# Kernel optimization log

Hardware: AMD Instinct MI355X
Metric: run time of the kernel (lower is better)

The kernel has to match this reference:

```python
import jax, jax.numpy as jnp
import numpy as np
import math

B, H, T, N = 2, 4, 2048, 2048
THETA = 2.0 ** 16


def get_freqs(n: int, theta: float) -> jnp.ndarray:
    # quantize arange to multiples of 2, matching torch (t/2).floor()*2
    t = jnp.arange(n, dtype=jnp.float32)
    q = jnp.floor(t / 2.0) * 2.0
    return 1.0 / theta ** (q / n) / (2.0 * math.pi)


def rope(phases: jnp.ndarray, v: jnp.ndarray) -> jnp.ndarray:
    # v: [B,H,T,N]; phases: [T,N] (broadcast). Interleaved pair rotation.
    ph = (phases % 1.0) * (2.0 * math.pi)
    c, s = jnp.cos(ph), jnp.sin(ph)
    v2 = v.reshape(*v.shape[:-1], -1, 2)           # [...,N/2,2]
    v_rot = jnp.stack((-v2[..., 1], v2[..., 0]), axis=-1).reshape(v.shape)
    return (v * c + v_rot * s).astype(v.dtype)


def setup_inputs() -> dict:
    key = jax.random.key(0)
    kq, kv = jax.random.split(key)
    Q = jax.random.normal(kq, (B, H, T, N), dtype=jnp.float32)
    V = jax.random.normal(kv, (B, H, T, N), dtype=jnp.float32)
    return {"Q": Q, "V": V}


def reference(Q, V):
    Tlen = Q.shape[2]
    n = Q.shape[3]
    freqs = get_freqs(n, THETA)                               # [N]
    phases = jnp.arange(Tlen, dtype=jnp.float32)[:, None] * freqs[None, :]  # [T,N]
    QR = rope(phases, Q)                                      # K is Q -> KR = QR
    scores = jnp.einsum('bhtn,bhsn->bhts', QR, QR)            # [B,H,T,T]
    # strictly-causal mask: keep s < t (tril with diagonal=-1)
    mask = jnp.tril(jnp.ones((Tlen, Tlen), dtype=bool), k=-1)
    scores = jnp.where(mask, scores, 0.0)
    out = jnp.einsum('bhts,bhsn->bhtn', scores, V)
    return out
```

## Files before the change

### kernel.cpp

```cpp
#include <hip/hip_runtime.h>
#include <hip/hip_bf16.h>

#define TDIM 2048
#define NDIM 2048
#define BHN  8
#define LD   2048

typedef __attribute__((ext_vector_type(8))) short bf16x8;
typedef __attribute__((ext_vector_type(4))) float f32x4;
typedef unsigned short us;

template <int N> struct ic { static constexpr int v = N; };

static __device__ __forceinline__ us f2bf(float x) {
  union { __hip_bfloat16 h; us u; } cv;
  cv.h = __float2bfloat16(x);
  return cv.u;
}

__global__ __launch_bounds__(256) void rope_kernel(const float* __restrict__ Q,
                                                   us* __restrict__ QR,
                                                   int total8) {
  int idx = blockIdx.x * blockDim.x + threadIdx.x;
  if (idx >= total8) return;
  long base = (long)idx * 8;
  int n = (int)(base & (NDIM - 1));
  int t = (int)((base >> 11) & (TDIM - 1));
  const float4* p = reinterpret_cast<const float4*>(Q + base);
  float4 v0 = p[0], v1 = p[1];
  float q[8] = {v0.x, v0.y, v0.z, v0.w, v1.x, v1.y, v1.z, v1.w};
  us r[8];
  float tf = (float)t;
#pragma unroll
  for (int pr = 0; pr < 4; ++pr) {
    int nn = n + pr * 2;
    float freq = __builtin_exp2f((float)nn * (-1.0f / 128.0f)) * 0.15915494309189535f;
    float ph = tf * freq;
    ph = ph - __builtin_floorf(ph);
    float c = __builtin_amdgcn_cosf(ph);
    float s = __builtin_amdgcn_sinf(ph);
    float e = q[2 * pr], o = q[2 * pr + 1];
    r[2 * pr]     = f2bf(e * c - o * s);
    r[2 * pr + 1] = f2bf(o * c + e * s);
  }
  union { us usv[8]; bf16x8 v; } pk;
#pragma unroll
  for (int i = 0; i < 8; ++i) pk.usv[i] = r[i];
  *reinterpret_cast<bf16x8*>(QR + base) = pk.v;
}

__global__ __launch_bounds__(256) void vtrans_kernel(const float* __restrict__ V,
                                                     us* __restrict__ VT,
                                                     us* __restrict__ Sflag) {
  __shared__ float tile[64 * 66];
  if (Sflag != nullptr && blockIdx.x == 0 && blockIdx.y == 0 && blockIdx.z == 0 &&
      threadIdx.x == 0) {
    for (int h = 0; h < BHN; ++h) {
      unsigned* f = (unsigned*)(Sflag + (long)h * TDIM * LD + 1792);
      for (int i = 0; i < 40; ++i)
        __hip_atomic_store(&f[i], 0u, __ATOMIC_RELAXED, __HIP_MEMORY_SCOPE_AGENT);
    }
  }
  const int bh = blockIdx.z;
  const int t0 = blockIdx.x * 64, n0 = blockIdx.y * 64;
  const float* Vp = V + (long)bh * TDIM * NDIM;
  us* Tp = VT + (long)bh * TDIM * NDIM;
  const int tid = (int)threadIdx.x;
  {
    const int tx4 = tid & 15, ty = tid >> 4;
#pragma unroll
    for (int i = 0; i < 4; ++i) {
      int row = ty + i * 16;
      float4 v = *reinterpret_cast<const float4*>(
          Vp + (long)(t0 + row) * NDIM + n0 + tx4 * 4);
      float* d = &tile[row * 66 + tx4 * 4];
      d[0] = v.x; d[1] = v.y; d[2] = v.z; d[3] = v.w;
    }
  }
  __syncthreads();
  {
    const int sx = tid & 15, sy = tid >> 4;
#pragma unroll
    for (int j = 0; j < 4; ++j) {
      int n = sy * 4 + j;
      unsigned r0 = f2bf(tile[(sx * 4 + 0) * 66 + n]);
      unsigned r1 = f2bf(tile[(sx * 4 + 1) * 66 + n]);
      unsigned r2 = f2bf(tile[(sx * 4 + 2) * 66 + n]);
      unsigned r3 = f2bf(tile[(sx * 4 + 3) * 66 + n]);
      uint2 val;
      val.x = r0 | (r1 << 16);
      val.y = r2 | (r3 << 16);
      *reinterpret_cast<uint2*>(Tp + (long)(n0 + n) * TDIM + t0 + sx * 4) = val;
    }
  }
}

template <int PASS>
__device__ __forceinline__ void run_tile(const us* __restrict__ A,
                                         const us* __restrict__ B,
                                         void* __restrict__ Cbase,
                                         us* __restrict__ lds,
                                         int rt, int ct, int tid,
                                         unsigned* __restrict__ fh) {
  const int lane = tid & 63, wid = tid >> 6;
  const int wr = wid >> 2, wc = wid & 3;
  const int l15 = lane & 15, l4 = lane >> 4;
  const int row0 = rt * 256, col0 = ct * 256;
  const int kts = (PASS == 0) ? 32 : (rt + 1) * 4;
  const int fbase = rt * (rt + 1) / 2;

  f32x4 acc[8][4];
#pragma unroll
  for (int m = 0; m < 8; ++m)
#pragma unroll
    for (int n = 0; n < 4; ++n) acc[m][n] = (f32x4){0.f, 0.f, 0.f, 0.f};

  auto stage = [&](int half , int t) {
    const us* g0 = (half < 2) ? A : B;
    const int tr0 = (half < 2) ? row0 : col0;
    const int h = half & 1;
    us* lb = lds + ((half < 2) ? 0 : 32768) + (t & 1) * 16384;
    const int k0 = t * 64;
#pragma unroll
    for (int r = 0; r < 2; ++r) {
      int off = r * 512 + tid;
      int row = off >> 3;
      int ch = off & 7;
      int chl = ch ^ (row & 7);
      const us* g = g0 + (long)(tr0 + h * 128 + row) * LD + (k0 + chl * 8);
      us* l = lb + h * 8192 + off * 8;
      __builtin_amdgcn_global_load_lds(
          (const __attribute__((address_space(1))) unsigned int*)g,
          (__attribute__((address_space(3))) unsigned int*)l, 16, 0, 0);
    }
  };
  auto ldA = [&](int b, int m, int ks) -> bf16x8 {
    int row = wr * 128 + m * 16 + l15;
    int ch = (ks * 4 + l4) ^ (row & 7);
    return *reinterpret_cast<const bf16x8*>(lds + b * 16384 + row * 64 + ch * 8);
  };
  auto ldB = [&](int b, int n, int ks) -> bf16x8 {
    int row = wc * 64 + n * 16 + l15;
    int ch = (ks * 4 + l4) ^ (row & 7);
    return *reinterpret_cast<const bf16x8*>(lds + 32768 + b * 16384 + row * 64 + ch * 8);
  };

  if constexpr (PASS == 1) {
    stage(2, 0); stage(3, 0);
    if (wid == 0) {
      unsigned need = (1u << (rt + 1)) - 1u;
      for (;;) {
        unsigned ok = 0;
        if (lane <= rt)
          ok = (__hip_atomic_fetch_add(&fh[fbase + lane], 0u, __ATOMIC_RELAXED,
                                       __HIP_MEMORY_SCOPE_AGENT) != 0u);
        unsigned long long m = __ballot(ok);
        if (((unsigned)m & need) == need) break;
        __builtin_amdgcn_s_sleep(8);
      }
    }
    __builtin_amdgcn_s_barrier();
    asm volatile("" ::: "memory");
    stage(0, 0); stage(1, 0);
    if (1 < kts) { stage(2, 1); stage(3, 1); }
  } else {
    stage(0, 0); stage(1, 0); stage(2, 0); stage(3, 0);
    if (1 < kts) { stage(2, 1); stage(3, 1); }
  }
  asm volatile("s_waitcnt vmcnt(4)" ::: "memory");
  __builtin_amdgcn_s_barrier();
  __builtin_amdgcn_sched_barrier(0);

  bf16x8 af[4][2], bfr[4][2];
  auto kstep = [&](int t, auto bbc) {
    constexpr int b = decltype(bbc)::v;
#pragma unroll
    for (int m = 0; m < 4; ++m) { af[m][0] = ldA(b, m, 0); af[m][1] = ldA(b, m, 1); }
#pragma unroll
    for (int n = 0; n < 2; ++n) { bfr[n][0] = ldB(b, n, 0); bfr[n][1] = ldB(b, n, 1); }
    if (t + 1 < kts) stage(0, t + 1);
    __builtin_amdgcn_s_barrier();
    asm volatile("s_waitcnt lgkmcnt(0)" ::: "memory");
    __builtin_amdgcn_sched_barrier(0);
    __builtin_amdgcn_s_setprio(1);
#pragma unroll
    for (int m = 0; m < 4; ++m)
#pragma unroll
      for (int n = 0; n < 2; ++n)
#pragma unroll
        for (int ks = 0; ks < 2; ++ks)
          acc[m][n] = __builtin_amdgcn_mfma_f32_16x16x32_bf16(af[m][ks], bfr[n][ks], acc[m][n], 0, 0, 0);
    __builtin_amdgcn_s_setprio(0);
    __builtin_amdgcn_sched_barrier(0);
    __builtin_amdgcn_s_barrier();
#pragma unroll
    for (int n = 2; n < 4; ++n) { bfr[n][0] = ldB(b, n, 0); bfr[n][1] = ldB(b, n, 1); }
    if (t + 1 < kts) stage(1, t + 1);
    __builtin_amdgcn_s_barrier();
    asm volatile("s_waitcnt lgkmcnt(0)" ::: "memory");
    __builtin_amdgcn_sched_barrier(0);
    __builtin_amdgcn_s_setprio(1);
#pragma unroll
    for (int m = 0; m < 4; ++m)
#pragma unroll
      for (int n = 2; n < 4; ++n)
#pragma unroll
        for (int ks = 0; ks < 2; ++ks)
          acc[m][n] = __builtin_amdgcn_mfma_f32_16x16x32_bf16(af[m][ks], bfr[n][ks], acc[m][n], 0, 0, 0);
    __builtin_amdgcn_s_setprio(0);
    __builtin_amdgcn_sched_barrier(0);
    __builtin_amdgcn_s_barrier();
#pragma unroll
    for (int m = 0; m < 4; ++m) { af[m][0] = ldA(b, m + 4, 0); af[m][1] = ldA(b, m + 4, 1); }
    if (t + 2 < kts) stage(2, t + 2);
    __builtin_amdgcn_s_barrier();
    asm volatile("s_waitcnt lgkmcnt(0)" ::: "memory");
    __builtin_amdgcn_sched_barrier(0);
    __builtin_amdgcn_s_setprio(1);
#pragma unroll
    for (int m = 0; m < 4; ++m)
#pragma unroll
      for (int n = 0; n < 2; ++n)
#pragma unroll
        for (int ks = 0; ks < 2; ++ks)
          acc[m + 4][n] = __builtin_amdgcn_mfma_f32_16x16x32_bf16(af[m][ks], bfr[n][ks], acc[m + 4][n], 0, 0, 0);
    __builtin_amdgcn_s_setprio(0);
    __builtin_amdgcn_sched_barrier(0);
    __builtin_amdgcn_s_barrier();
    if (t + 2 < kts) stage(3, t + 2);
    __builtin_amdgcn_s_setprio(1);
#pragma unroll
    for (int m = 0; m < 4; ++m)
#pragma unroll
      for (int n = 2; n < 4; ++n)
#pragma unroll
        for (int ks = 0; ks < 2; ++ks)
          acc[m + 4][n] = __builtin_amdgcn_mfma_f32_16x16x32_bf16(af[m][ks], bfr[n][ks], acc[m + 4][n], 0, 0, 0);
    __builtin_amdgcn_s_setprio(0);
    if (t + 2 < kts) { asm volatile("s_waitcnt vmcnt(4)" ::: "memory"); }
    else             { asm volatile("s_waitcnt vmcnt(0)" ::: "memory"); }
    __builtin_amdgcn_sched_barrier(0);
    __builtin_amdgcn_s_barrier();
    __builtin_amdgcn_sched_barrier(0);
  };
  for (int t = 0; t < kts; t += 2) {
    kstep(t, ic<0>{});
    kstep(t + 1, ic<1>{});
  }

  if constexpr (PASS == 0) {
    us* C = (us*)Cbase;
    const bool diag = (rt == ct);
#pragma unroll
    for (int m = 0; m < 8; ++m) {
      int r0 = row0 + wr * 128 + m * 16 + l4 * 4;
#pragma unroll
      for (int n = 0; n < 4; ++n) {
        int cc = col0 + wc * 64 + n * 16 + l15;
#pragma unroll
        for (int j = 0; j < 4; ++j) {
          int tt = r0 + j;
          float v = acc[m][n][j];
          if (diag && cc >= tt) v = 0.0f;
          C[(long)tt * LD + cc] = f2bf(v);
        }
      }
    }
    __syncthreads();
    if (tid == 0)
      __hip_atomic_store(&fh[fbase + ct], 1u, __ATOMIC_RELEASE,
                         __HIP_MEMORY_SCOPE_AGENT);
  } else {
    float* C = (float*)Cbase;
#pragma unroll
    for (int m = 0; m < 8; ++m) {
      int r0 = row0 + wr * 128 + m * 16 + l4 * 4;
#pragma unroll
      for (int n = 0; n < 4; ++n) {
        int cc = col0 + wc * 64 + n * 16 + l15;
#pragma unroll
        for (int j = 0; j < 4; ++j)
          C[(long)(r0 + j) * LD + cc] = acc[m][n][j];
      }
    }
  }
}

__global__ __launch_bounds__(512, 2) void gemm_fused(const us* __restrict__ QR,
                                                     const us* __restrict__ VT,
                                                     us* __restrict__ S,
                                                     float* __restrict__ Out) {
  extern __shared__ us lds[];
  const int b = (int)blockIdx.x;
  const int head = b & 7, u = b >> 3;
  const int tid = (int)threadIdx.x;
  const us* QRh = QR + (long)head * TDIM * LD;
  const us* VTh = VT + (long)head * TDIM * LD;
  us* Sh = S + (long)head * TDIM * LD;
  float* Oh = Out + (long)head * TDIM * LD;
  unsigned* fh = (unsigned*)(Sh + 1792);
  unsigned* qc = fh + 36;

  int rt0, ct0;
  if (u < 8)       { rt0 = 7; ct0 = u; }
  else if (u < 15) { rt0 = 6; ct0 = u - 8; }
  else if (u < 21) { rt0 = 5; ct0 = u - 15; }
  else if (u < 26) { rt0 = 4; ct0 = u - 21; }
  else if (u < 30) { rt0 = 3; ct0 = u - 26; }
  else             { rt0 = 2; ct0 = (u == 30) ? 0 : 2; }
  run_tile<0>(QRh, QRh, Sh, lds, rt0, ct0, tid, fh);
  if (u >= 28) {
    int rt1, ct1;
    if (u == 28)      { rt1 = 1; ct1 = 0; }
    else if (u == 29) { rt1 = 1; ct1 = 1; }
    else if (u == 30) { rt1 = 2; ct1 = 1; }
    else              { rt1 = 0; ct1 = 0; }
    run_tile<0>(QRh, QRh, Sh, lds, rt1, ct1, tid, fh);
    run_tile<1>(Sh, VTh, Oh, lds, 1, u - 28, tid, fh);
  }

  for (;;) {
    if (tid == 0) {
      unsigned i = __hip_atomic_fetch_add(qc, 1u, __ATOMIC_RELAXED,
                                          __HIP_MEMORY_SCOPE_AGENT);
      *(volatile unsigned*)lds = i;
    }
    __syncthreads();
    unsigned i = *(volatile unsigned*)lds;
    __syncthreads();
    if (i >= 60) break;
    int rt, ct;
    if (i < 48)      { rt = 7 - (int)(i >> 3); ct = (int)(i & 7); }
    else if (i < 52) { rt = 1; ct = (int)(i - 44); }
    else             { rt = 0; ct = (int)(i - 52); }
    run_tile<1>(Sh, VTh, Oh, lds, rt, ct, tid, fh);
  }
}

template <int PASS>
__global__ __launch_bounds__(512, 2) void gemm256(
    const us* __restrict__ Abase, const us* __restrict__ Bbase,
    void* __restrict__ Cbase, int nh) {
  extern __shared__ us lds[];
  int bid = (int)blockIdx.x;
  int head, rt = 0, ct, cls = 0;
  if constexpr (PASS == 0) {
    head = bid % nh;
    int tri = bid / nh;
    rt = 0;
    while ((rt + 1) * (rt + 2) / 2 <= tri) ++rt;
    ct = tri - rt * (rt + 1) / 2;
  } else {
    head = bid % nh;
    int rem = bid / nh;
    ct = rem & 7;
    cls = rem >> 3;
  }
  const us* A = Abase + (long)head * TDIM * LD;
  const us* B = Bbase + (long)head * TDIM * LD;
  us* Sh = (us*)Cbase + (long)head * TDIM * LD;
  const int tid = (int)threadIdx.x;
  const int NSEG = (PASS == 0) ? 1 : 2;
#pragma unroll 1
  for (int seg = 0; seg < NSEG; ++seg) {
    int rts = rt, cts = ct;
    if constexpr (PASS == 1) { rts = seg ? cls : 7 - cls; cts = ct; }
    if constexpr (PASS == 0) {
      run_tile<0>(A, A, Sh, lds, rts, cts, tid, (unsigned*)(Sh + 1792));
    } else {
      float* Oh = (float*)Cbase + (long)head * TDIM * LD;
      run_tile<1>(A, B, Oh, lds, rts, cts, tid,
                  (unsigned*)((us*)Abase + (long)head * TDIM * LD + 1792));
    }
  }
}

extern "C" void kernel_launch(void* const* d_in, const int* in_sizes, int n_in,
                              void* d_out, int out_size, void* d_ws, size_t ws_size,
                              hipStream_t stream) {
  const float* Q = (const float*)d_in[0];
  const float* V = (const float*)d_in[1];
  float* Out = (float*)d_out;
  char* ws = (char*)d_ws;
  const long TN = (long)TDIM * NDIM;
  const size_t BUF = (size_t)BHN * TN * 2;
  const size_t PERBH = (size_t)TN * 2;
  const int SHMEM = 131072;

  hipFuncSetAttribute(reinterpret_cast<const void*>(&gemm_fused),
                      hipFuncAttributeMaxDynamicSharedMemorySize, SHMEM);
  hipFuncSetAttribute(reinterpret_cast<const void*>(&gemm256<0>),
                      hipFuncAttributeMaxDynamicSharedMemorySize, SHMEM);
  hipFuncSetAttribute(reinterpret_cast<const void*>(&gemm256<1>),
                      hipFuncAttributeMaxDynamicSharedMemorySize, SHMEM);

  if (ws_size >= 3 * BUF) {
    us* QRb = (us*)ws;
    us* VbT = (us*)(ws + BUF);
    us* S   = (us*)(ws + 2 * BUF);
    int total8 = (int)(BHN * TN / 8);
    rope_kernel<<<dim3(total8 / 256), dim3(256), 0, stream>>>(Q, QRb, total8);
    vtrans_kernel<<<dim3(32, 32, 8), dim3(256), 0, stream>>>(V, VbT, S);
    void* args[] = {(void*)&QRb, (void*)&VbT, (void*)&S, (void*)&Out};
    hipError_t ce = hipLaunchCooperativeKernel(
        reinterpret_cast<const void*>(&gemm_fused), dim3(256), dim3(512),
        args, (unsigned)SHMEM, stream);
    if (ce != hipSuccess) {
      (void)hipGetLastError();
      gemm256<0><<<dim3(36 * BHN), dim3(512), SHMEM, stream>>>(QRb, QRb, S, BHN);
      gemm256<1><<<dim3(32 * BHN), dim3(512), SHMEM, stream>>>(S, VbT, Out, BHN);
    }
  } else {
    us* QR0 = (us*)ws;
    us* VT0 = (us*)(ws + PERBH);
    us* S0  = (us*)(ws + 2 * PERBH);
    int total8 = (int)(TN / 8);
    for (int bh = 0; bh < BHN; ++bh) {
      rope_kernel<<<dim3(total8 / 256), dim3(256), 0, stream>>>(Q + bh * TN, QR0, total8);
      vtrans_kernel<<<dim3(32, 32, 1), dim3(256), 0, stream>>>(V + bh * TN, VT0, S0);
      gemm256<0><<<dim3(36), dim3(512), SHMEM, stream>>>(QR0, QR0, S0, 1);
      gemm256<1><<<dim3(32), dim3(512), SHMEM, stream>>>(S0, VT0, Out + bh * TN, 1);
    }
  }
}
```

Before: 280.2 us.

## Prefetch work-queue index during tile and move flag wait before staging

The persistent PV loop now fetches the next work-queue index with an atomic while the current tile runs. The index is stored in a dedicated LDS slot, which grows shared memory by 16 bytes, so the atomic latency is hidden behind compute. The dependency-flag spin wait for pass 1 moves to the start of the tile, so the V-tile prefetch no longer overlaps the wait. The k-loop is also rewritten from a compile-time double-buffer lambda into a runtime loop that uses `t & 1` as the buffer index. This drops constant-folded LDS addressing and may add address arithmetic.

```diff
diff --git a/kernel.cpp b/kernel.cpp
--- a/kernel.cpp
+++ b/kernel.cpp
@@ -9,8 +9,6 @@
 typedef __attribute__((ext_vector_type(8))) short bf16x8;
 typedef __attribute__((ext_vector_type(4))) float f32x4;
 typedef unsigned short us;
-
-template <int N> struct ic { static constexpr int v = N; };
 
 static __device__ __forceinline__ us f2bf(float x) {
   union { __hip_bfloat16 h; us u; } cv;
@@ -109,6 +107,23 @@
   const int kts = (PASS == 0) ? 32 : (rt + 1) * 4;
   const int fbase = rt * (rt + 1) / 2;
 
+  if constexpr (PASS == 1) {
+    if (wid == 0) {
+      unsigned need = (1u << (rt + 1)) - 1u;
+      for (;;) {
+        unsigned ok = 0;
+        if (lane <= rt)
+          ok = (__hip_atomic_fetch_add(&fh[fbase + lane], 0u, __ATOMIC_RELAXED,
+                                       __HIP_MEMORY_SCOPE_AGENT) != 0u);
+        unsigned long long m = __ballot(ok);
+        if (((unsigned)m & need) == need) break;
+        __builtin_amdgcn_s_sleep(8);
+      }
+    }
+    __builtin_amdgcn_s_barrier();
+    asm volatile("" ::: "memory");
+  }
+
   f32x4 acc[8][4];
 #pragma unroll
   for (int m = 0; m < 8; ++m)
@@ -145,35 +160,15 @@
     return *reinterpret_cast<const bf16x8*>(lds + 32768 + b * 16384 + row * 64 + ch * 8);
   };
 
-  if constexpr (PASS == 1) {
-    stage(2, 0); stage(3, 0);
-    if (wid == 0) {
-      unsigned need = (1u << (rt + 1)) - 1u;
-      for (;;) {
-        unsigned ok = 0;
-        if (lane <= rt)
-          ok = (__hip_atomic_fetch_add(&fh[fbase + lane], 0u, __ATOMIC_RELAXED,
-                                       __HIP_MEMORY_SCOPE_AGENT) != 0u);
-        unsigned long long m = __ballot(ok);
-        if (((unsigned)m & need) == need) break;
-        __builtin_amdgcn_s_sleep(8);
-      }
-    }
-    __builtin_amdgcn_s_barrier();
-    asm volatile("" ::: "memory");
-    stage(0, 0); stage(1, 0);
-    if (1 < kts) { stage(2, 1); stage(3, 1); }
-  } else {
-    stage(0, 0); stage(1, 0); stage(2, 0); stage(3, 0);
-    if (1 < kts) { stage(2, 1); stage(3, 1); }
-  }
+  stage(0, 0); stage(1, 0); stage(2, 0); stage(3, 0);
+  if (1 < kts) { stage(2, 1); stage(3, 1); }
   asm volatile("s_waitcnt vmcnt(4)" ::: "memory");
   __builtin_amdgcn_s_barrier();
   __builtin_amdgcn_sched_barrier(0);
 
   bf16x8 af[4][2], bfr[4][2];
-  auto kstep = [&](int t, auto bbc) {
-    constexpr int b = decltype(bbc)::v;
+  for (int t = 0; t < kts; ++t) {
+    const int b = t & 1;
 #pragma unroll
     for (int m = 0; m < 4; ++m) { af[m][0] = ldA(b, m, 0); af[m][1] = ldA(b, m, 1); }
 #pragma unroll
@@ -242,10 +237,6 @@
     __builtin_amdgcn_sched_barrier(0);
     __builtin_amdgcn_s_barrier();
     __builtin_amdgcn_sched_barrier(0);
-  };
-  for (int t = 0; t < kts; t += 2) {
-    kstep(t, ic<0>{});
-    kstep(t + 1, ic<1>{});
   }
 
   if constexpr (PASS == 0) {
@@ -300,6 +291,7 @@
   float* Oh = Out + (long)head * TDIM * LD;
   unsigned* fh = (unsigned*)(Sh + 1792);
   unsigned* qc = fh + 36;
+  volatile unsigned* qslot = (volatile unsigned*)(lds + 65536);
 
   int rt0, ct0;
   if (u < 8)       { rt0 = 7; ct0 = u; }
@@ -319,21 +311,28 @@
     run_tile<1>(Sh, VTh, Oh, lds, 1, u - 28, tid, fh);
   }
 
-  for (;;) {
+  if (tid == 0) {
+    unsigned i = __hip_atomic_fetch_add(qc, 1u, __ATOMIC_RELAXED,
+                                        __HIP_MEMORY_SCOPE_AGENT);
+    *qslot = i;
+  }
+  __syncthreads();
+  unsigned icur = *qslot;
+  __syncthreads();
+  while (icur < 60) {
     if (tid == 0) {
       unsigned i = __hip_atomic_fetch_add(qc, 1u, __ATOMIC_RELAXED,
                                           __HIP_MEMORY_SCOPE_AGENT);
-      *(volatile unsigned*)lds = i;
-    }
+      *qslot = i;
+    }
+    int rt, ct;
+    if (icur < 48)      { rt = 7 - (int)(icur >> 3); ct = (int)(icur & 7); }
+    else if (icur < 52) { rt = 1; ct = (int)(icur - 44); }
+    else                { rt = 0; ct = (int)(icur - 52); }
+    run_tile<1>(Sh, VTh, Oh, lds, rt, ct, tid, fh);
     __syncthreads();
-    unsigned i = *(volatile unsigned*)lds;
+    icur = *qslot;
     __syncthreads();
-    if (i >= 60) break;
-    int rt, ct;
-    if (i < 48)      { rt = 7 - (int)(i >> 3); ct = (int)(i & 7); }
-    else if (i < 52) { rt = 1; ct = (int)(i - 44); }
-    else             { rt = 0; ct = (int)(i - 52); }
-    run_tile<1>(Sh, VTh, Oh, lds, rt, ct, tid, fh);
   }
 }
 
@@ -385,7 +384,7 @@
   const long TN = (long)TDIM * NDIM;
   const size_t BUF = (size_t)BHN * TN * 2;
   const size_t PERBH = (size_t)TN * 2;
-  const int SHMEM = 131072;
+  const int SHMEM = 131088;
 
   hipFuncSetAttribute(reinterpret_cast<const void*>(&gemm_fused),
                       hipFuncAttributeMaxDynamicSharedMemorySize, SHMEM);
```

Result: no change. 282.6 us (+0.9%).

## Merge rope and V-transpose into one prep kernel and simplify GEMM k-loop

Applied to the files above, without the earlier changes.

Combines the rope and V-transpose kernels into a single prep launch that dispatches blocks by index, removing one launch and the gap between them. In the GEMM tile, the pass-1 flag wait now happens before any staging instead of overlapping with the B-tile prefetch. The manually unrolled two-step kstep lambda with compile-time buffer index is also replaced by a plain loop with a runtime buffer index. The later flag wait and runtime LDS indexing may cost some latency hiding and add address arithmetic.

```diff
diff --git a/kernel.cpp b/kernel.cpp
--- a/kernel.cpp
+++ b/kernel.cpp
@@ -10,20 +10,15 @@
 typedef __attribute__((ext_vector_type(4))) float f32x4;
 typedef unsigned short us;
 
-template <int N> struct ic { static constexpr int v = N; };
-
 static __device__ __forceinline__ us f2bf(float x) {
   union { __hip_bfloat16 h; us u; } cv;
   cv.h = __float2bfloat16(x);
   return cv.u;
 }
 
-__global__ __launch_bounds__(256) void rope_kernel(const float* __restrict__ Q,
-                                                   us* __restrict__ QR,
-                                                   int total8) {
-  int idx = blockIdx.x * blockDim.x + threadIdx.x;
-  if (idx >= total8) return;
-  long base = (long)idx * 8;
+static __device__ __forceinline__ void rope_unit(const float* __restrict__ Q,
+                                                 us* __restrict__ QR, long idx) {
+  long base = idx * 8;
   int n = (int)(base & (NDIM - 1));
   int t = (int)((base >> 11) & (TDIM - 1));
   const float4* p = reinterpret_cast<const float4*>(Q + base);
@@ -49,23 +44,10 @@
   *reinterpret_cast<bf16x8*>(QR + base) = pk.v;
 }
 
-__global__ __launch_bounds__(256) void vtrans_kernel(const float* __restrict__ V,
-                                                     us* __restrict__ VT,
-                                                     us* __restrict__ Sflag) {
-  __shared__ float tile[64 * 66];
-  if (Sflag != nullptr && blockIdx.x == 0 && blockIdx.y == 0 && blockIdx.z == 0 &&
-      threadIdx.x == 0) {
-    for (int h = 0; h < BHN; ++h) {
-      unsigned* f = (unsigned*)(Sflag + (long)h * TDIM * LD + 1792);
-      for (int i = 0; i < 40; ++i)
-        __hip_atomic_store(&f[i], 0u, __ATOMIC_RELAXED, __HIP_MEMORY_SCOPE_AGENT);
-    }
-  }
-  const int bh = blockIdx.z;
-  const int t0 = blockIdx.x * 64, n0 = blockIdx.y * 64;
-  const float* Vp = V + (long)bh * TDIM * NDIM;
-  us* Tp = VT + (long)bh * TDIM * NDIM;
-  const int tid = (int)threadIdx.x;
+static __device__ __forceinline__ void vtrans_tile(const float* __restrict__ Vp,
+                                                   us* __restrict__ Tp,
+                                                   float* __restrict__ tile,
+                                                   int t0, int n0, int tid) {
   {
     const int tx4 = tid & 15, ty = tid >> 4;
 #pragma unroll
@@ -93,6 +75,34 @@
       *reinterpret_cast<uint2*>(Tp + (long)(n0 + n) * TDIM + t0 + sx * 4) = val;
     }
   }
+}
+
+__global__ __launch_bounds__(256) void prep_kernel(const float* __restrict__ Q,
+                                                   const float* __restrict__ V,
+                                                   us* __restrict__ QR,
+                                                   us* __restrict__ VT,
+                                                   us* __restrict__ Sflag,
+                                                   int nh) {
+  __shared__ float tile[64 * 66];
+  const int bid = (int)blockIdx.x;
+  const int tid = (int)threadIdx.x;
+  const int nrope = nh * 2048;
+  if (bid == 0 && tid == 0) {
+    for (int h = 0; h < nh; ++h) {
+      unsigned* f = (unsigned*)(Sflag + (long)h * TDIM * LD + 1792);
+      for (int i = 0; i < 40; ++i)
+        __hip_atomic_store(&f[i], 0u, __ATOMIC_RELAXED, __HIP_MEMORY_SCOPE_AGENT);
+    }
+  }
+  if (bid < nrope) {
+    rope_unit(Q, QR, (long)bid * 256 + tid);
+    return;
+  }
+  const int vb = bid - nrope;
+  const int bh = vb >> 10;
+  const int rem = vb & 1023;
+  vtrans_tile(V + (long)bh * TDIM * NDIM, VT + (long)bh * TDIM * NDIM, tile,
+              (rem & 31) * 64, (rem >> 5) * 64, tid);
 }
 
 template <int PASS>
@@ -109,6 +119,23 @@
   const int kts = (PASS == 0) ? 32 : (rt + 1) * 4;
   const int fbase = rt * (rt + 1) / 2;
 
+  if constexpr (PASS == 1) {
+    if (wid == 0) {
+      unsigned need = (1u << (rt + 1)) - 1u;
+      for (;;) {
+        unsigned ok = 0;
+        if (lane <= rt)
+          ok = (__hip_atomic_fetch_add(&fh[fbase + lane], 0u, __ATOMIC_RELAXED,
+                                       __HIP_MEMORY_SCOPE_AGENT) != 0u);
+        unsigned long long m = __ballot(ok);
+        if (((unsigned)m & need) == need) break;
+        __builtin_amdgcn_s_sleep(8);
+      }
+    }
+    __builtin_amdgcn_s_barrier();
+    asm volatile("" ::: "memory");
+  }
+
   f32x4 acc[8][4];
 #pragma unroll
   for (int m = 0; m < 8; ++m)
@@ -145,35 +172,15 @@
     return *reinterpret_cast<const bf16x8*>(lds + 32768 + b * 16384 + row * 64 + ch * 8);
   };
 
-  if constexpr (PASS == 1) {
-    stage(2, 0); stage(3, 0);
-    if (wid == 0) {
-      unsigned need = (1u << (rt + 1)) - 1u;
-      for (;;) {
-        unsigned ok = 0;
-        if (lane <= rt)
-          ok = (__hip_atomic_fetch_add(&fh[fbase + lane], 0u, __ATOMIC_RELAXED,
-                                       __HIP_MEMORY_SCOPE_AGENT) != 0u);
-        unsigned long long m = __ballot(ok);
-        if (((unsigned)m & need) == need) break;
-        __builtin_amdgcn_s_sleep(8);
-      }
-    }
-    __builtin_amdgcn_s_barrier();
-    asm volatile("" ::: "memory");
-    stage(0, 0); stage(1, 0);
-    if (1 < kts) { stage(2, 1); stage(3, 1); }
-  } else {
-    stage(0, 0); stage(1, 0); stage(2, 0); stage(3, 0);
-    if (1 < kts) { stage(2, 1); stage(3, 1); }
-  }
+  stage(0, 0); stage(1, 0); stage(2, 0); stage(3, 0);
+  if (1 < kts) { stage(2, 1); stage(3, 1); }
   asm volatile("s_waitcnt vmcnt(4)" ::: "memory");
   __builtin_amdgcn_s_barrier();
   __builtin_amdgcn_sched_barrier(0);
 
   bf16x8 af[4][2], bfr[4][2];
-  auto kstep = [&](int t, auto bbc) {
-    constexpr int b = decltype(bbc)::v;
+  for (int t = 0; t < kts; ++t) {
+    const int b = t & 1;
 #pragma unroll
     for (int m = 0; m < 4; ++m) { af[m][0] = ldA(b, m, 0); af[m][1] = ldA(b, m, 1); }
 #pragma unroll
@@ -242,10 +249,6 @@
     __builtin_amdgcn_sched_barrier(0);
     __builtin_amdgcn_s_barrier();
     __builtin_amdgcn_sched_barrier(0);
-  };
-  for (int t = 0; t < kts; t += 2) {
-    kstep(t, ic<0>{});
-    kstep(t + 1, ic<1>{});
   }
 
   if constexpr (PASS == 0) {
@@ -398,9 +401,7 @@
     us* QRb = (us*)ws;
     us* VbT = (us*)(ws + BUF);
     us* S   = (us*)(ws + 2 * BUF);
-    int total8 = (int)(BHN * TN / 8);
-    rope_kernel<<<dim3(total8 / 256), dim3(256), 0, stream>>>(Q, QRb, total8);
-    vtrans_kernel<<<dim3(32, 32, 8), dim3(256), 0, stream>>>(V, VbT, S);
+    prep_kernel<<<dim3(BHN * 3072), dim3(256), 0, stream>>>(Q, V, QRb, VbT, S, BHN);
     void* args[] = {(void*)&QRb, (void*)&VbT, (void*)&S, (void*)&Out};
     hipError_t ce = hipLaunchCooperativeKernel(
         reinterpret_cast<const void*>(&gemm_fused), dim3(256), dim3(512),
@@ -414,10 +415,9 @@
     us* QR0 = (us*)ws;
     us* VT0 = (us*)(ws + PERBH);
     us* S0  = (us*)(ws + 2 * PERBH);
-    int total8 = (int)(TN / 8);
     for (int bh = 0; bh < BHN; ++bh) {
-      rope_kernel<<<dim3(total8 / 256), dim3(256), 0, stream>>>(Q + bh * TN, QR0, total8);
-      vtrans_kernel<<<dim3(32, 32, 1), dim3(256), 0, stream>>>(V + bh * TN, VT0, S0);
+      prep_kernel<<<dim3(3072), dim3(256), 0, stream>>>(
+          Q + bh * TN, V + bh * TN, QR0, VT0, S0, 1);
       gemm256<0><<<dim3(36), dim3(512), SHMEM, stream>>>(QR0, QR0, S0, 1);
       gemm256<1><<<dim3(32), dim3(512), SHMEM, stream>>>(S0, VT0, Out + bh * TN, 1);
     }
```

New measurement: 258.8 us. 7.6% less time.
